# Kernel tuning notes

Hardware: AMD Instinct MI355X
Metric: run time of the kernel (lower is better)

Reference implementation:

```python
import jax, jax.numpy as jnp
import numpy as np

N_NODES = 50000
N_EDGES = 800000
HIDDEN = 128
MLP_DIM = 64

def setup_inputs() -> dict:
    key = jax.random.key(0)
    k1, k2, k3, k4 = jax.random.split(key, 4)
    node_emb = jax.random.normal(k1, (N_NODES, HIDDEN), dtype=jnp.float32)
    edge_index = jax.random.randint(k2, (2, N_EDGES), 0, N_NODES, dtype=jnp.int64)
    # Xavier-uniform init like the torch module
    lim1 = float(np.sqrt(6.0 / (2 * HIDDEN + MLP_DIM)))
    lim2 = float(np.sqrt(6.0 / (MLP_DIM + 1)))
    W1 = jax.random.uniform(k3, (2 * HIDDEN, MLP_DIM), minval=-lim1, maxval=lim1, dtype=jnp.float32)
    b1 = jnp.zeros((MLP_DIM,), dtype=jnp.float32)
    W2 = jax.random.uniform(k4, (MLP_DIM, 1), minval=-lim2, maxval=lim2, dtype=jnp.float32)
    b2 = jnp.zeros((1,), dtype=jnp.float32)
    return {"node_emb": node_emb, "edge_index": edge_index, "W1": W1, "b1": b1, "W2": W2, "b2": b2}

def reference(node_emb, edge_index, W1, b1, W2, b2):
    src, dst = edge_index[0], edge_index[1]
    emb_src = node_emb[src]                      # [E, H] gather
    emb_dst = node_emb[dst]                      # [E, H] gather
    edge_emb = jnp.concatenate([emb_src, emb_dst], axis=1)  # [E, 2H]
    h = jax.nn.relu(edge_emb @ W1 + b1)          # [E, MLP_DIM]
    edge_logits = h @ W2 + b2                    # [E, 1]
    return edge_logits
```

## Files before the change

### kernel.cpp

```cpp
#include <hip/hip_runtime.h>
#include <hip/hip_bf16.h>


#define HIDDEN 128

typedef __attribute__((ext_vector_type(8))) short bf16x8;
typedef __attribute__((ext_vector_type(4))) float f32x4;
typedef __attribute__((ext_vector_type(8))) _Float16 half8;

__device__ inline unsigned short f32_to_bf16(float f) {
    unsigned int u = __float_as_uint(f);
    unsigned int r = (u + 0x7fffu + ((u >> 16) & 1u)) >> 16;
    return (unsigned short)r;
}

__global__ __launch_bounds__(256, 2) void precompute_pq_mfma(
    const float* __restrict__ node_emb,
    const float* __restrict__ W1,
    const float* __restrict__ b1,
    _Float16* __restrict__ PQ,
    int n_nodes)
{
    __shared__ unsigned short Bt[128 * 136];
    __shared__ _Float16 Out[64 * 136];

    const int t = threadIdx.x;
    const int wave = t >> 6, lane = t & 63;
    const int lrow = lane & 15;
    const int kq = (lane >> 4) * 8;
    const int m0 = blockIdx.x * 64;
    const int m = m0 + wave * 16 + lrow;
    const bool valid = (m < n_nodes);

    const float* arow = node_emb + (size_t)(valid ? m : 0) * HIDDEN + kq;
    float4 aLo[4], aHi[4];
    #pragma unroll
    for (int i = 0; i < 4; ++i) {
        if (valid) {
            aLo[i] = *(const float4*)(arow + i * 32);
            aHi[i] = *(const float4*)(arow + i * 32 + 4);
        } else {
            aLo[i] = make_float4(0.f, 0.f, 0.f, 0.f);
            aHi[i] = aLo[i];
        }
    }

    #pragma unroll
    for (int it = 0; it < 16; ++it) {
        int slot = it * 256 + t;
        int r = slot >> 4;
        int c4 = (slot & 15) * 4;
        float4 v = *(const float4*)&W1[r * 64 + c4];
        int j = (r < 128) ? c4 : (c4 + 64);
        int k = r & 127;
        Bt[(j + 0) * 136 + k] = f32_to_bf16(v.x);
        Bt[(j + 1) * 136 + k] = f32_to_bf16(v.y);
        Bt[(j + 2) * 136 + k] = f32_to_bf16(v.z);
        Bt[(j + 3) * 136 + k] = f32_to_bf16(v.w);
    }
    __syncthreads();

    f32x4 acc[8];
    #pragma unroll
    for (int c = 0; c < 8; ++c) acc[c] = (f32x4){0.f, 0.f, 0.f, 0.f};

    #pragma unroll
    for (int k0i = 0; k0i < 4; ++k0i) {
        union { bf16x8 v; __hip_bfloat162 h[4]; } ua;
        ua.h[0] = __float22bfloat162_rn(make_float2(aLo[k0i].x, aLo[k0i].y));
        ua.h[1] = __float22bfloat162_rn(make_float2(aLo[k0i].z, aLo[k0i].w));
        ua.h[2] = __float22bfloat162_rn(make_float2(aHi[k0i].x, aHi[k0i].y));
        ua.h[3] = __float22bfloat162_rn(make_float2(aHi[k0i].z, aHi[k0i].w));
        const int kbase = k0i * 32 + kq;
        #pragma unroll
        for (int c = 0; c < 8; ++c) {
            bf16x8 bf = *(const bf16x8*)&Bt[(c * 16 + lrow) * 136 + kbase];
            acc[c] = __builtin_amdgcn_mfma_f32_16x16x32_bf16(ua.v, bf, acc[c], 0, 0, 0);
        }
    }

    const int rbase = (lane >> 4) * 4;
    #pragma unroll
    for (int c = 0; c < 8; ++c) {
        int col = c * 16 + lrow;
        float bias = (col < 64) ? b1[col] : 0.f;
        #pragma unroll
        for (int reg = 0; reg < 4; ++reg) {
            int row = wave * 16 + rbase + reg;
            Out[row * 136 + col] = (_Float16)(acc[c][reg] + bias);
        }
    }
    __syncthreads();
    #pragma unroll
    for (int i = 0; i < 4; ++i) {
        int idx = i * 256 + t;
        int row = idx >> 4;
        int cg = (idx & 15) * 8;
        int mm = m0 + row;
        if (mm < n_nodes) {
            half8 v = *(const half8*)&Out[row * 136 + cg];
            *(half8*)&PQ[(size_t)mm * HIDDEN + cg] = v;
        }
    }
}

__global__ __launch_bounds__(256, 4) void edge_mlp16(
    const _Float16* __restrict__ PQ,
    const int* __restrict__ edge_index,
    const float* __restrict__ W2,
    const float* __restrict__ b2,
    float* __restrict__ out,
    int E)
{
    const int t = threadIdx.x;
    const int g = t & 7;
    const int slot = t >> 3;
    const int e0 = blockIdx.x * 64 + slot;
    const int e1 = e0 + 32;

    float4 wA = *(const float4*)&W2[g * 8];
    float4 wB = *(const float4*)&W2[g * 8 + 4];

    const bool v0 = e0 < E, v1 = e1 < E;
    int src0 = 0, dst0 = 0, src1 = 0, dst1 = 0;
    if (v0) { src0 = edge_index[e0]; dst0 = edge_index[E + e0]; }
    if (v1) { src1 = edge_index[e1]; dst1 = edge_index[E + e1]; }

    half8 p0{}, q0{}, p1{}, q1{};
    if (v0) {
        p0 = *(const half8*)&PQ[(size_t)src0 * HIDDEN + g * 8];
        q0 = *(const half8*)&PQ[(size_t)dst0 * HIDDEN + 64 + g * 8];
    }
    if (v1) {
        p1 = *(const half8*)&PQ[(size_t)src1 * HIDDEN + g * 8];
        q1 = *(const half8*)&PQ[(size_t)dst1 * HIDDEN + 64 + g * 8];
    }

    float s0 = 0.f, s1 = 0.f;
    s0 += fmaxf((float)p0[0] + (float)q0[0], 0.f) * wA.x;
    s0 += fmaxf((float)p0[1] + (float)q0[1], 0.f) * wA.y;
    s0 += fmaxf((float)p0[2] + (float)q0[2], 0.f) * wA.z;
    s0 += fmaxf((float)p0[3] + (float)q0[3], 0.f) * wA.w;
    s0 += fmaxf((float)p0[4] + (float)q0[4], 0.f) * wB.x;
    s0 += fmaxf((float)p0[5] + (float)q0[5], 0.f) * wB.y;
    s0 += fmaxf((float)p0[6] + (float)q0[6], 0.f) * wB.z;
    s0 += fmaxf((float)p0[7] + (float)q0[7], 0.f) * wB.w;

    s1 += fmaxf((float)p1[0] + (float)q1[0], 0.f) * wA.x;
    s1 += fmaxf((float)p1[1] + (float)q1[1], 0.f) * wA.y;
    s1 += fmaxf((float)p1[2] + (float)q1[2], 0.f) * wA.z;
    s1 += fmaxf((float)p1[3] + (float)q1[3], 0.f) * wA.w;
    s1 += fmaxf((float)p1[4] + (float)q1[4], 0.f) * wB.x;
    s1 += fmaxf((float)p1[5] + (float)q1[5], 0.f) * wB.y;
    s1 += fmaxf((float)p1[6] + (float)q1[6], 0.f) * wB.z;
    s1 += fmaxf((float)p1[7] + (float)q1[7], 0.f) * wB.w;

    s0 += __shfl_xor(s0, 1, 64);  s1 += __shfl_xor(s1, 1, 64);
    s0 += __shfl_xor(s0, 2, 64);  s1 += __shfl_xor(s1, 2, 64);
    s0 += __shfl_xor(s0, 4, 64);  s1 += __shfl_xor(s1, 4, 64);

    if (g == 0) {
        float bb = b2[0];
        if (v0) out[e0] = s0 + bb;
        if (v1) out[e1] = s1 + bb;
    }
}

extern "C" void kernel_launch(void* const* d_in, const int* in_sizes, int n_in,
                              void* d_out, int out_size, void* d_ws, size_t ws_size,
                              hipStream_t stream) {
    const float* node_emb   = (const float*)d_in[0];
    const int*   edge_index = (const int*)d_in[1];
    const float* W1 = (const float*)d_in[2];
    const float* b1 = (const float*)d_in[3];
    const float* W2 = (const float*)d_in[4];
    const float* b2 = (const float*)d_in[5];
    float* out = (float*)d_out;

    const int n_nodes = in_sizes[0] / HIDDEN;
    const int E = in_sizes[1] / 2;

    _Float16* PQ = (_Float16*)d_ws;

    const int grid1 = (n_nodes + 63) / 64;
    precompute_pq_mfma<<<grid1, 256, 0, stream>>>(node_emb, W1, b1, PQ, n_nodes);

    const int grid2 = (E + 63) / 64;
    edge_mlp16<<<grid2, 256, 0, stream>>>(PQ, edge_index, W2, b2, out, E);
}
```

Before: 115.2 us.

## Write PQ directly from MFMA registers and drop edge bounds checks

```diff
diff --git a/kernel.cpp b/kernel.cpp
--- a/kernel.cpp
+++ b/kernel.cpp
@@ -7,6 +7,7 @@
 typedef __attribute__((ext_vector_type(8))) short bf16x8;
 typedef __attribute__((ext_vector_type(4))) float f32x4;
 typedef __attribute__((ext_vector_type(8))) _Float16 half8;
+typedef __attribute__((ext_vector_type(4))) _Float16 half4f;
 
 __device__ inline unsigned short f32_to_bf16(float f) {
     unsigned int u = __float_as_uint(f);
@@ -14,7 +15,7 @@
     return (unsigned short)r;
 }
 
-__global__ __launch_bounds__(256, 2) void precompute_pq_mfma(
+__global__ __launch_bounds__(256, 4) void precompute_pq_mfma(
     const float* __restrict__ node_emb,
     const float* __restrict__ W1,
     const float* __restrict__ b1,
@@ -22,17 +23,16 @@
     int n_nodes)
 {
     __shared__ unsigned short Bt[128 * 136];
-    __shared__ _Float16 Out[64 * 136];
 
     const int t = threadIdx.x;
     const int wave = t >> 6, lane = t & 63;
-    const int lrow = lane & 15;
+    const int l15 = lane & 15;
     const int kq = (lane >> 4) * 8;
     const int m0 = blockIdx.x * 64;
-    const int m = m0 + wave * 16 + lrow;
-    const bool valid = (m < n_nodes);
+    const int node = m0 + wave * 16 + l15;
+    const bool valid = (node < n_nodes);
 
-    const float* arow = node_emb + (size_t)(valid ? m : 0) * HIDDEN + kq;
+    const float* arow = node_emb + (size_t)(valid ? node : 0) * HIDDEN + kq;
     float4 aLo[4], aHi[4];
     #pragma unroll
     for (int i = 0; i < 4; ++i) {
@@ -74,37 +74,36 @@
         const int kbase = k0i * 32 + kq;
         #pragma unroll
         for (int c = 0; c < 8; ++c) {
-            bf16x8 bf = *(const bf16x8*)&Bt[(c * 16 + lrow) * 136 + kbase];
-            acc[c] = __builtin_amdgcn_mfma_f32_16x16x32_bf16(ua.v, bf, acc[c], 0, 0, 0);
+            bf16x8 wf = *(const bf16x8*)&Bt[(c * 16 + l15) * 136 + kbase];
+            acc[c] = __builtin_amdgcn_mfma_f32_16x16x32_bf16(wf, ua.v, acc[c], 0, 0, 0);
         }
     }
 
-    const int rbase = (lane >> 4) * 4;
-    #pragma unroll
-    for (int c = 0; c < 8; ++c) {
-        int col = c * 16 + lrow;
-        float bias = (col < 64) ? b1[col] : 0.f;
+    if (valid) {
+        const int rbase = (lane >> 4) * 4;
+        float4 bias[4];
         #pragma unroll
-        for (int reg = 0; reg < 4; ++reg) {
-            int row = wave * 16 + rbase + reg;
-            Out[row * 136 + col] = (_Float16)(acc[c][reg] + bias);
-        }
-    }
-    __syncthreads();
-    #pragma unroll
-    for (int i = 0; i < 4; ++i) {
-        int idx = i * 256 + t;
-        int row = idx >> 4;
-        int cg = (idx & 15) * 8;
-        int mm = m0 + row;
-        if (mm < n_nodes) {
-            half8 v = *(const half8*)&Out[row * 136 + cg];
-            *(half8*)&PQ[(size_t)mm * HIDDEN + cg] = v;
+        for (int c = 0; c < 4; ++c) bias[c] = *(const float4*)&b1[c * 16 + rbase];
+        _Float16* drow = PQ + (size_t)node * HIDDEN;
+        #pragma unroll
+        for (int c = 0; c < 8; ++c) {
+            half4f v;
+            if (c < 4) {
+                const float* bf = (const float*)&bias[c];
+                #pragma unroll
+                for (int reg = 0; reg < 4; ++reg)
+                    v[reg] = (_Float16)(acc[c][reg] + bf[reg]);
+            } else {
+                #pragma unroll
+                for (int reg = 0; reg < 4; ++reg)
+                    v[reg] = (_Float16)acc[c][reg];
+            }
+            *(half4f*)&drow[c * 16 + rbase] = v;
         }
     }
 }
 
-__global__ __launch_bounds__(256, 4) void edge_mlp16(
+__global__ __launch_bounds__(256) void edge_mlp16(
     const _Float16* __restrict__ PQ,
     const int* __restrict__ edge_index,
     const float* __restrict__ W2,
@@ -121,39 +120,29 @@
     float4 wA = *(const float4*)&W2[g * 8];
     float4 wB = *(const float4*)&W2[g * 8 + 4];
 
-    const bool v0 = e0 < E, v1 = e1 < E;
-    int src0 = 0, dst0 = 0, src1 = 0, dst1 = 0;
-    if (v0) { src0 = edge_index[e0]; dst0 = edge_index[E + e0]; }
-    if (v1) { src1 = edge_index[e1]; dst1 = edge_index[E + e1]; }
+    const int src0 = __builtin_nontemporal_load(&edge_index[e0]);
+    const int dst0 = __builtin_nontemporal_load(&edge_index[E + e0]);
+    const int src1 = __builtin_nontemporal_load(&edge_index[e1]);
+    const int dst1 = __builtin_nontemporal_load(&edge_index[E + e1]);
 
-    half8 p0{}, q0{}, p1{}, q1{};
-    if (v0) {
-        p0 = *(const half8*)&PQ[(size_t)src0 * HIDDEN + g * 8];
-        q0 = *(const half8*)&PQ[(size_t)dst0 * HIDDEN + 64 + g * 8];
+    half8 p0 = *(const half8*)&PQ[(size_t)src0 * HIDDEN + g * 8];
+    half8 q0 = *(const half8*)&PQ[(size_t)dst0 * HIDDEN + 64 + g * 8];
+    half8 p1 = *(const half8*)&PQ[(size_t)src1 * HIDDEN + g * 8];
+    half8 q1 = *(const half8*)&PQ[(size_t)dst1 * HIDDEN + 64 + g * 8];
+
+    const float* wa = (const float*)&wA;
+    const float* wb = (const float*)&wB;
+    float s0 = 0.f, s1 = 0.f;
+    #pragma unroll
+    for (int i = 0; i < 4; ++i) {
+        s0 = fmaf(fmaxf((float)p0[i] + (float)q0[i], 0.f), wa[i], s0);
+        s1 = fmaf(fmaxf((float)p1[i] + (float)q1[i], 0.f), wa[i], s1);
     }
-    if (v1) {
-        p1 = *(const half8*)&PQ[(size_t)src1 * HIDDEN + g * 8];
-        q1 = *(const half8*)&PQ[(size_t)dst1 * HIDDEN + 64 + g * 8];
+    #pragma unroll
+    for (int i = 0; i < 4; ++i) {
+        s0 = fmaf(fmaxf((float)p0[i + 4] + (float)q0[i + 4], 0.f), wb[i], s0);
+        s1 = fmaf(fmaxf((float)p1[i + 4] + (float)q1[i + 4], 0.f), wb[i], s1);
     }
-
-    float s0 = 0.f, s1 = 0.f;
-    s0 += fmaxf((float)p0[0] + (float)q0[0], 0.f) * wA.x;
-    s0 += fmaxf((float)p0[1] + (float)q0[1], 0.f) * wA.y;
-    s0 += fmaxf((float)p0[2] + (float)q0[2], 0.f) * wA.z;
-    s0 += fmaxf((float)p0[3] + (float)q0[3], 0.f) * wA.w;
-    s0 += fmaxf((float)p0[4] + (float)q0[4], 0.f) * wB.x;
-    s0 += fmaxf((float)p0[5] + (float)q0[5], 0.f) * wB.y;
-    s0 += fmaxf((float)p0[6] + (float)q0[6], 0.f) * wB.z;
-    s0 += fmaxf((float)p0[7] + (float)q0[7], 0.f) * wB.w;
-
-    s1 += fmaxf((float)p1[0] + (float)q1[0], 0.f) * wA.x;
-    s1 += fmaxf((float)p1[1] + (float)q1[1], 0.f) * wA.y;
-    s1 += fmaxf((float)p1[2] + (float)q1[2], 0.f) * wA.z;
-    s1 += fmaxf((float)p1[3] + (float)q1[3], 0.f) * wA.w;
-    s1 += fmaxf((float)p1[4] + (float)q1[4], 0.f) * wB.x;
-    s1 += fmaxf((float)p1[5] + (float)q1[5], 0.f) * wB.y;
-    s1 += fmaxf((float)p1[6] + (float)q1[6], 0.f) * wB.z;
-    s1 += fmaxf((float)p1[7] + (float)q1[7], 0.f) * wB.w;
 
     s0 += __shfl_xor(s0, 1, 64);  s1 += __shfl_xor(s1, 1, 64);
     s0 += __shfl_xor(s0, 2, 64);  s1 += __shfl_xor(s1, 2, 64);
@@ -161,8 +150,8 @@
 
     if (g == 0) {
         float bb = b2[0];
-        if (v0) out[e0] = s0 + bb;
-        if (v1) out[e1] = s1 + bb;
+        __builtin_nontemporal_store(s0 + bb, &out[e0]);
+        __builtin_nontemporal_store(s1 + bb, &out[e1]);
     }
 }
 
@@ -185,6 +174,6 @@
     const int grid1 = (n_nodes + 63) / 64;
     precompute_pq_mfma<<<grid1, 256, 0, stream>>>(node_emb, W1, b1, PQ, n_nodes);
 
-    const int grid2 = (E + 63) / 64;
+    const int grid2 = E / 64;
     edge_mlp16<<<grid2, 256, 0, stream>>>(PQ, edge_index, W2, b2, out, E);
 }
```

Result: no change. 114.8 us (-0.3%).
